# Optimization experiments

Measured on AMD Instinct MI355X. Metric: run time of the kernel, lower is better.

Reference implementation:

```python
import jax, jax.numpy as jnp
import numpy as np

DIM = 1024


def setup_inputs() -> dict:
    key = jax.random.key(0)
    ks = jax.random.split(key, 10)
    B, S, D = 8, 2048, DIM
    sd = 1.0 / np.sqrt(D)  # nn.Linear default init scale
    return {
        "query": jax.random.normal(ks[0], (B, S, D), jnp.float32),
        "key": jax.random.normal(ks[1], (B, S, D), jnp.float32),
        "value": jax.random.normal(ks[2], (B, S, D), jnp.float32),
        "context": jnp.zeros((D,), jnp.float32),
        "Wq": jax.random.uniform(ks[3], (D, D), jnp.float32, -sd, sd),
        "bq": jax.random.uniform(ks[4], (D,), jnp.float32, -sd, sd),
        "Wk": jax.random.uniform(ks[5], (D, D), jnp.float32, -sd, sd),
        "bk": jax.random.uniform(ks[6], (D,), jnp.float32, -sd, sd),
        "Wv": jax.random.uniform(ks[7], (D, D), jnp.float32, -sd, sd),
        "bv": jax.random.uniform(ks[8], (D,), jnp.float32, -sd, sd),
    }


def reference(query, key, value, context, Wq, bq, Wk, bk, Wv, bv):
    D = query.shape[-1]
    scale = D ** (-0.5)
    # context bias added to inputs BEFORE q/k projections (not v)
    q = jnp.einsum("bsd,ed->bse", query + context, Wq) + bq
    k = jnp.einsum("bsd,ed->bse", key + context, Wk) + bk
    v = jnp.einsum("bsd,ed->bse", value, Wv) + bv
    scores = jnp.einsum("bqd,bkd->bqk", q, k) * scale  # [B,S,S]
    S = scores.shape[-1]
    causal = jnp.triu(jnp.ones((S, S), jnp.bool_), k=1)  # True = masked
    scores = jnp.where(causal, -jnp.inf, scores)
    weights = jax.nn.softmax(scores, axis=-1)
    out = jnp.einsum("bqk,bkd->bqd", weights, v)
    return out
```

## Files before the change

kernel.cpp:

```cpp
#include <hip/hip_runtime.h>
#include <hip/hip_bf16.h>
#include <stdint.h>
#include <math.h>

#define DIM   1024
#define SEQ   2048
#define BATCH 8
#define BSD   (BATCH * SEQ * DIM)
#define DD    (DIM * DIM)

typedef __attribute__((ext_vector_type(8))) short short8;
typedef __attribute__((ext_vector_type(4))) float floatx4;
typedef unsigned int u32;
typedef unsigned short ushort_t;

#define GLOAD_LDS16(gptr, lptr)                                                   \
    __builtin_amdgcn_global_load_lds(                                             \
        (const __attribute__((address_space(1))) u32*)(gptr),                     \
        (__attribute__((address_space(3))) u32*)(lptr), 16, 0, 0)

__device__ __forceinline__ uint2 pack4bf(float a, float b, float c, float d) {
    union { __hip_bfloat162 h; unsigned u; } p0, p1;
    p0.h = __float22bfloat162_rn(float2{a, b});
    p1.h = __float22bfloat162_rn(float2{c, d});
    return uint2{p0.u, p1.u};
}

__global__ __launch_bounds__(256) void convert_kernel(
    const float* __restrict__ q, const float* __restrict__ k, const float* __restrict__ v,
    const float* __restrict__ ctx,
    const float* __restrict__ Wq, const float* __restrict__ Wk, const float* __restrict__ Wv,
    ushort_t* __restrict__ xq, ushort_t* __restrict__ xk, ushort_t* __restrict__ xv,
    ushort_t* __restrict__ wq, ushort_t* __restrict__ wk, ushort_t* __restrict__ wv)
{
    const long idx = (long)blockIdx.x * 256 + threadIdx.x;
    const long T  = BSD / 4;
    const long W4 = DD / 4;
    if (idx < 3 * T) {
        const int  seg = (int)(idx >> 22);
        const long off = idx & (T - 1);
        const float* src = (seg == 0) ? q : (seg == 1) ? k : v;
        ushort_t*    dst = (seg == 0) ? xq : (seg == 1) ? xk : xv;
        float4 x = ((const float4*)src)[off];
        if (seg < 2) {
            const float4 c = ((const float4*)ctx)[off & (DIM / 4 - 1)];
            x.x += c.x; x.y += c.y; x.z += c.z; x.w += c.w;
        }
        ((uint2*)dst)[off] = pack4bf(x.x, x.y, x.z, x.w);
    } else {
        const long r   = idx - 3 * T;
        const int  seg = (int)(r >> 18);
        const long off = r & (W4 - 1);
        const float* src = (seg == 0) ? Wq : (seg == 1) ? Wk : Wv;
        ushort_t*    dst = (seg == 0) ? wq : (seg == 1) ? wk : wv;
        const float4 x = ((const float4*)src)[off];
        ((uint2*)dst)[off] = pack4bf(x.x, x.y, x.z, x.w);
    }
}

__global__ __launch_bounds__(256) void gemm_bf16(
    const ushort_t* __restrict__ X, const ushort_t* __restrict__ W,
    const float* __restrict__ bias, ushort_t* __restrict__ out, int transpose_out)
{
    __shared__ ushort_t As[128 * 64];
    __shared__ ushort_t Bs[128 * 64];

    const int tid  = threadIdx.x;
    const int lane = tid & 63;
    const int wave = tid >> 6;
    const int quad = lane >> 4;
    const int l16  = lane & 15;
    const int wy = wave >> 1, wx = wave & 1;
    const int row0 = blockIdx.x * 128;
    const int col0 = blockIdx.y * 128;

    floatx4 acc[4][4];
#pragma unroll
    for (int i = 0; i < 4; ++i)
#pragma unroll
        for (int j = 0; j < 4; ++j)
            acc[i][j] = (floatx4){0.f, 0.f, 0.f, 0.f};

    const int srow = lane >> 3;
    const int scol = (lane & 7) * 8;

    for (int k0 = 0; k0 < DIM; k0 += 64) {
#pragma unroll
        for (int i = 0; i < 4; ++i) {
            const int slot = wave * 4 + i;
            const int grow = slot * 8 + srow;
            GLOAD_LDS16(&X[(size_t)(row0 + grow) * DIM + k0 + scol],
                        &As[slot * 512 + lane * 8]);
            GLOAD_LDS16(&W[(size_t)(col0 + grow) * DIM + k0 + scol],
                        &Bs[slot * 512 + lane * 8]);
        }
        __syncthreads();

        short8 af[4][2], bfr[4][2];
#pragma unroll
        for (int t = 0; t < 4; ++t)
#pragma unroll
            for (int ks = 0; ks < 2; ++ks) {
                af[t][ks]  = *(const short8*)&As[(wy * 64 + t * 16 + l16) * 64 + ks * 32 + quad * 8];
                bfr[t][ks] = *(const short8*)&Bs[(wx * 64 + t * 16 + l16) * 64 + ks * 32 + quad * 8];
            }
#pragma unroll
        for (int ks = 0; ks < 2; ++ks)
#pragma unroll
            for (int mt = 0; mt < 4; ++mt)
#pragma unroll
                for (int nt = 0; nt < 4; ++nt)
                    acc[mt][nt] = __builtin_amdgcn_mfma_f32_16x16x32_bf16(
                        af[mt][ks], bfr[nt][ks], acc[mt][nt], 0, 0, 0);
        __syncthreads();
    }

#pragma unroll
    for (int nt = 0; nt < 4; ++nt) {
        const int n = col0 + wx * 64 + nt * 16 + l16;
        const float bz = bias[n];
#pragma unroll
        for (int mt = 0; mt < 4; ++mt) {
            const int mbase = row0 + wy * 64 + mt * 16 + quad * 4;
            const floatx4 a = acc[mt][nt];
            if (!transpose_out) {
#pragma unroll
                for (int rg = 0; rg < 4; ++rg) {
                    union { __hip_bfloat16 h; ushort_t u; } cv;
                    cv.h = __float2bfloat16(a[rg] + bz);
                    out[(size_t)(mbase + rg) * DIM + n] = cv.u;
                }
            } else {
                const int bb = mbase >> 11;
                const int ss = mbase & (SEQ - 1);
                *(uint2*)&out[((size_t)bb * DIM + n) * SEQ + ss] =
                    pack4bf(a[0] + bz, a[1] + bz, a[2] + bz, a[3] + bz);
            }
        }
    }
}

__global__ __launch_bounds__(512, 2) void attn_kernel(
    const ushort_t* __restrict__ Q, const ushort_t* __restrict__ K,
    const ushort_t* __restrict__ VT, float* __restrict__ out)
{
    __shared__ float Sp[8 * 32 * 36];
    __shared__ ushort_t Pl[32 * 72];
    __shared__ float mS[32], lS[32], aS[32];

    const int tid  = threadIdx.x;
    const int lane = tid & 63;
    const int wave = tid >> 6;
    const int quad = lane >> 4;
    const int l16  = lane & 15;

    const int jt = wave >> 2;
    const int dq = wave & 3;
    const int d0 = dq * 256;

    const int by = blockIdx.x & 7;
    const int p  = blockIdx.x >> 3;

    const size_t qrow = (size_t)by * SEQ;
    const size_t vrow = (size_t)by * DIM;
    const int dchunk = wave * 128;

    const int rr  = tid >> 4;
    const int kt  = tid & 15;
    const int kk0 = kt * 4;
    const int sjt = kk0 >> 5;
    const int sc  = kk0 & 31;

    for (int pass = 0; pass < 2; ++pass) {
        const int t  = pass ? (63 - p) : p;
        const int q0 = t * 32;
        const int ngroups = (t + 2) >> 1;

        if (tid < 32) { mS[tid] = -INFINITY; lS[tid] = 0.f; aS[tid] = 0.f; }

        short8 qa[2][8];
#pragma unroll
        for (int mt = 0; mt < 2; ++mt)
#pragma unroll
            for (int ks = 0; ks < 8; ++ks)
                qa[mt][ks] = *(const short8*)
                    &Q[(qrow + q0 + mt * 16 + l16) * DIM + d0 + ks * 32 + quad * 8];

        floatx4 o[2][8];
#pragma unroll
        for (int mt = 0; mt < 2; ++mt)
#pragma unroll
            for (int nt = 0; nt < 8; ++nt)
                o[mt][nt] = (floatx4){0.f, 0.f, 0.f, 0.f};

        __syncthreads();

        for (int g = 0; g < ngroups; ++g) {
            const int k0 = g * 64 + jt * 32;

            floatx4 s00 = (floatx4){0.f,0.f,0.f,0.f}, s01 = s00, s10 = s00, s11 = s00;
            const ushort_t* kbp = &K[(qrow + k0 + l16) * DIM + d0 + quad * 8];
#pragma unroll
            for (int ks = 0; ks < 8; ++ks) {
                const short8 kb0 = *(const short8*)&kbp[ks * 32];
                const short8 kb1 = *(const short8*)&kbp[16 * DIM + ks * 32];
                s00 = __builtin_amdgcn_mfma_f32_16x16x32_bf16(qa[0][ks], kb0, s00, 0, 0, 0);
                s10 = __builtin_amdgcn_mfma_f32_16x16x32_bf16(qa[1][ks], kb0, s10, 0, 0, 0);
                s01 = __builtin_amdgcn_mfma_f32_16x16x32_bf16(qa[0][ks], kb1, s01, 0, 0, 0);
                s11 = __builtin_amdgcn_mfma_f32_16x16x32_bf16(qa[1][ks], kb1, s11, 0, 0, 0);
            }
#pragma unroll
            for (int rg = 0; rg < 4; ++rg) {
                const int r0 = quad * 4 + rg;
                Sp[(wave * 32 + r0) * 36 + l16]           = s00[rg];
                Sp[(wave * 32 + r0) * 36 + 16 + l16]      = s01[rg];
                Sp[(wave * 32 + 16 + r0) * 36 + l16]      = s10[rg];
                Sp[(wave * 32 + 16 + r0) * 36 + 16 + l16] = s11[rg];
            }
            __syncthreads();

            short8 vcur[8];
#pragma unroll
            for (int nt = 0; nt < 8; ++nt)
                vcur[nt] = *(const short8*)
                    &VT[(vrow + dchunk + nt * 16 + l16) * SEQ + g * 64 + quad * 8];

            float sv[4];
            {
                const float* a0 = &Sp[((sjt * 4 + 0) * 32 + rr) * 36 + sc];
                const float4 x0 = *(const float4*)&a0[0];
                const float4 x1 = *(const float4*)&a0[32 * 36];
                const float4 x2 = *(const float4*)&a0[2 * 32 * 36];
                const float4 x3 = *(const float4*)&a0[3 * 32 * 36];
                sv[0] = x0.x + x1.x + x2.x + x3.x;
                sv[1] = x0.y + x1.y + x2.y + x3.y;
                sv[2] = x0.z + x1.z + x2.z + x3.z;
                sv[3] = x0.w + x1.w + x2.w + x3.w;
            }
            const int rowg = q0 + rr;
#pragma unroll
            for (int i = 0; i < 4; ++i) {
                const int key = g * 64 + kk0 + i;
                sv[i] = (key > rowg) ? -INFINITY : sv[i] * 0.03125f;
            }
            float mx = fmaxf(fmaxf(sv[0], sv[1]), fmaxf(sv[2], sv[3]));
#pragma unroll
            for (int off = 1; off < 16; off <<= 1) mx = fmaxf(mx, __shfl_xor(mx, off));
            const float mold = mS[rr];
            const float mnew = fmaxf(mold, mx);
            const float p0 = __expf(sv[0] - mnew), p1 = __expf(sv[1] - mnew);
            const float p2 = __expf(sv[2] - mnew), p3 = __expf(sv[3] - mnew);
            float rs = (p0 + p1) + (p2 + p3);
#pragma unroll
            for (int off = 1; off < 16; off <<= 1) rs += __shfl_xor(rs, off);
            const float alpha = __expf(mold - mnew);
            if (kt == 0) {
                mS[rr] = mnew;
                lS[rr] = lS[rr] * alpha + rs;
                aS[rr] = alpha;
            }
            *(uint2*)&Pl[rr * 72 + kk0] = pack4bf(p0, p1, p2, p3);
            __syncthreads();

#pragma unroll
            for (int mt = 0; mt < 2; ++mt) {
                const float a0 = aS[mt * 16 + quad * 4 + 0];
                const float a1 = aS[mt * 16 + quad * 4 + 1];
                const float a2 = aS[mt * 16 + quad * 4 + 2];
                const float a3 = aS[mt * 16 + quad * 4 + 3];
#pragma unroll
                for (int nt = 0; nt < 8; ++nt) {
                    o[mt][nt][0] *= a0; o[mt][nt][1] *= a1;
                    o[mt][nt][2] *= a2; o[mt][nt][3] *= a3;
                }
            }
            {
                const short8 pa0 = *(const short8*)&Pl[l16 * 72 + quad * 8];
                const short8 pa1 = *(const short8*)&Pl[(16 + l16) * 72 + quad * 8];
#pragma unroll
                for (int nt = 0; nt < 8; ++nt) {
                    o[0][nt] = __builtin_amdgcn_mfma_f32_16x16x32_bf16(pa0, vcur[nt], o[0][nt], 0, 0, 0);
                    o[1][nt] = __builtin_amdgcn_mfma_f32_16x16x32_bf16(pa1, vcur[nt], o[1][nt], 0, 0, 0);
                }
            }
            {
                short8 vb[8];
#pragma unroll
                for (int nt = 0; nt < 8; ++nt)
                    vb[nt] = *(const short8*)
                        &VT[(vrow + dchunk + nt * 16 + l16) * SEQ + g * 64 + 32 + quad * 8];
                const short8 pa0 = *(const short8*)&Pl[l16 * 72 + 32 + quad * 8];
                const short8 pa1 = *(const short8*)&Pl[(16 + l16) * 72 + 32 + quad * 8];
#pragma unroll
                for (int nt = 0; nt < 8; ++nt) {
                    o[0][nt] = __builtin_amdgcn_mfma_f32_16x16x32_bf16(pa0, vb[nt], o[0][nt], 0, 0, 0);
                    o[1][nt] = __builtin_amdgcn_mfma_f32_16x16x32_bf16(pa1, vb[nt], o[1][nt], 0, 0, 0);
                }
            }
        }

#pragma unroll
        for (int mt = 0; mt < 2; ++mt) {
            const float li0 = 1.f / lS[mt * 16 + quad * 4 + 0];
            const float li1 = 1.f / lS[mt * 16 + quad * 4 + 1];
            const float li2 = 1.f / lS[mt * 16 + quad * 4 + 2];
            const float li3 = 1.f / lS[mt * 16 + quad * 4 + 3];
#pragma unroll
            for (int nt = 0; nt < 8; ++nt) {
                const size_t base = (qrow + q0 + mt * 16 + quad * 4) * DIM + wave * 128 + nt * 16 + l16;
                out[base]           = o[mt][nt][0] * li0;
                out[base + DIM]     = o[mt][nt][1] * li1;
                out[base + 2 * DIM] = o[mt][nt][2] * li2;
                out[base + 3 * DIM] = o[mt][nt][3] * li3;
            }
        }
        __syncthreads();
    }
}

extern "C" void kernel_launch(void* const* d_in, const int* in_sizes, int n_in,
                              void* d_out, int out_size, void* d_ws, size_t ws_size,
                              hipStream_t stream) {
    const float* query = (const float*)d_in[0];
    const float* key   = (const float*)d_in[1];
    const float* value = (const float*)d_in[2];
    const float* ctx   = (const float*)d_in[3];
    const float* Wq    = (const float*)d_in[4];
    const float* bq    = (const float*)d_in[5];
    const float* Wk    = (const float*)d_in[6];
    const float* bk    = (const float*)d_in[7];
    const float* Wv    = (const float*)d_in[8];
    const float* bv    = (const float*)d_in[9];

    ushort_t* A = (ushort_t*)d_ws;
    ushort_t* B = A + (size_t)BSD;
    ushort_t* C = B + (size_t)BSD;
    ushort_t* D = C + (size_t)BSD;
    ushort_t* wqb = D + (size_t)BSD;
    ushort_t* wkb = wqb + (size_t)DD;
    ushort_t* wvb = wkb + (size_t)DD;
    float* out = (float*)d_out;

    {
        const long total = 3L * (BSD / 4) + 3L * (DD / 4);
        convert_kernel<<<dim3((unsigned)(total / 256)), dim3(256), 0, stream>>>(
            query, key, value, ctx, Wq, Wk, Wv, A, B, C, wqb, wkb, wvb);
    }

    const dim3 pg((BATCH * SEQ) / 128, DIM / 128);
    gemm_bf16<<<pg, dim3(256), 0, stream>>>(C, wvb, bv, D, 1);
    gemm_bf16<<<pg, dim3(256), 0, stream>>>(A, wqb, bq, C, 0);
    gemm_bf16<<<pg, dim3(256), 0, stream>>>(B, wkb, bk, A, 0);

    attn_kernel<<<dim3(BATCH * (SEQ / 64)), dim3(512), 0, stream>>>(C, A, D, out);
}
```

Measured before the change: 674.6 us.

## Split QK^T over all waves by head-dim and prefetch next K tile into registers

Each wave now computes the full 32x64 score tile over its own 128-wide slice of the head dimension, instead of a 32x32 half over a 256-wide slice. The eight partial tiles are summed through a larger LDS buffer. The K fragments for the next key group are loaded into a second register buffer, alternating between two buffers, while the current group runs, so global load latency overlaps with compute. The cost is more register pressure from the two 4x4 short8 K buffers under launch_bounds(512,2), plus twice the LDS reduction reads and a larger Sp array.

New measurement: 1.335 ms. 1.98x slower.

```diff
diff --git a/kernel.cpp b/kernel.cpp
--- a/kernel.cpp
+++ b/kernel.cpp
@@ -140,11 +140,114 @@
     }
 }
 
+#define ATTN_GROUP(G, KC, KN)                                                      \
+    {                                                                              \
+        floatx4 s[2][4];                                                           \
+        _Pragma("unroll")                                                          \
+        for (int mt = 0; mt < 2; ++mt)                                             \
+            _Pragma("unroll")                                                      \
+            for (int kf = 0; kf < 4; ++kf)                                         \
+                s[mt][kf] = (floatx4){0.f, 0.f, 0.f, 0.f};                         \
+        _Pragma("unroll")                                                          \
+        for (int ks = 0; ks < 4; ++ks)                                             \
+            _Pragma("unroll")                                                      \
+            for (int kf = 0; kf < 4; ++kf) {                                       \
+                s[0][kf] = __builtin_amdgcn_mfma_f32_16x16x32_bf16(qa[0][ks], KC[kf][ks], s[0][kf], 0, 0, 0); \
+                s[1][kf] = __builtin_amdgcn_mfma_f32_16x16x32_bf16(qa[1][ks], KC[kf][ks], s[1][kf], 0, 0, 0); \
+            }                                                                      \
+        _Pragma("unroll")                                                          \
+        for (int kf = 0; kf < 4; ++kf)                                             \
+            _Pragma("unroll")                                                      \
+            for (int rg = 0; rg < 4; ++rg) {                                       \
+                const int r0 = quad * 4 + rg;                                      \
+                Sp[(wave * 32 + r0) * 68 + kf * 16 + l16]      = s[0][kf][rg];     \
+                Sp[(wave * 32 + 16 + r0) * 68 + kf * 16 + l16] = s[1][kf][rg];     \
+            }                                                                      \
+        if ((G) + 1 < ngroups) {                                                   \
+            const ushort_t* knp = &K[(qrow + ((G) + 1) * 64 + l16) * DIM + d0 + quad * 8]; \
+            _Pragma("unroll")                                                      \
+            for (int kf = 0; kf < 4; ++kf)                                         \
+                _Pragma("unroll")                                                  \
+                for (int ks = 0; ks < 4; ++ks)                                     \
+                    KN[kf][ks] = *(const short8*)&knp[(size_t)kf * 16 * DIM + ks * 32]; \
+        }                                                                          \
+        __syncthreads();                                                           \
+        short8 vcur[8];                                                            \
+        _Pragma("unroll")                                                          \
+        for (int nt = 0; nt < 8; ++nt)                                             \
+            vcur[nt] = *(const short8*)&VT[(vrow + d0 + nt * 16 + l16) * SEQ + (G) * 64 + quad * 8]; \
+        float sv[4];                                                               \
+        {                                                                          \
+            const float* ap = &Sp[rr * 68 + kk0];                                  \
+            float4 acc4 = *(const float4*)&ap[0];                                  \
+            _Pragma("unroll")                                                      \
+            for (int w = 1; w < 8; ++w) {                                          \
+                const float4 x = *(const float4*)&ap[w * 32 * 68];                 \
+                acc4.x += x.x; acc4.y += x.y; acc4.z += x.z; acc4.w += x.w;        \
+            }                                                                      \
+            sv[0] = acc4.x; sv[1] = acc4.y; sv[2] = acc4.z; sv[3] = acc4.w;        \
+        }                                                                          \
+        const int rowg = q0 + rr;                                                  \
+        _Pragma("unroll")                                                          \
+        for (int i = 0; i < 4; ++i) {                                              \
+            const int key = (G) * 64 + kk0 + i;                                    \
+            sv[i] = (key > rowg) ? -INFINITY : sv[i] * 0.03125f;                   \
+        }                                                                          \
+        float mx = fmaxf(fmaxf(sv[0], sv[1]), fmaxf(sv[2], sv[3]));                \
+        _Pragma("unroll")                                                          \
+        for (int off = 1; off < 16; off <<= 1) mx = fmaxf(mx, __shfl_xor(mx, off)); \
+        const float mold = mS[rr];                                                 \
+        const float mnew = fmaxf(mold, mx);                                        \
+        const float p0 = __expf(sv[0] - mnew), p1 = __expf(sv[1] - mnew);          \
+        const float p2 = __expf(sv[2] - mnew), p3 = __expf(sv[3] - mnew);          \
+        float rsum = (p0 + p1) + (p2 + p3);                                        \
+        _Pragma("unroll")                                                          \
+        for (int off = 1; off < 16; off <<= 1) rsum += __shfl_xor(rsum, off);      \
+        const float alpha = __expf(mold - mnew);                                   \
+        if (kt == 0) { mS[rr] = mnew; lS[rr] = lS[rr] * alpha + rsum; aS[rr] = alpha; } \
+        *(uint2*)&Pl[rr * 72 + kk0] = pack4bf(p0, p1, p2, p3);                     \
+        __syncthreads();                                                           \
+        _Pragma("unroll")                                                          \
+        for (int mt = 0; mt < 2; ++mt) {                                           \
+            const float a0r = aS[mt * 16 + quad * 4 + 0];                          \
+            const float a1r = aS[mt * 16 + quad * 4 + 1];                          \
+            const float a2r = aS[mt * 16 + quad * 4 + 2];                          \
+            const float a3r = aS[mt * 16 + quad * 4 + 3];                          \
+            _Pragma("unroll")                                                      \
+            for (int nt = 0; nt < 8; ++nt) {                                       \
+                o[mt][nt][0] *= a0r; o[mt][nt][1] *= a1r;                          \
+                o[mt][nt][2] *= a2r; o[mt][nt][3] *= a3r;                          \
+            }                                                                      \
+        }                                                                          \
+        {                                                                          \
+            const short8 pa0 = *(const short8*)&Pl[l16 * 72 + quad * 8];           \
+            const short8 pa1 = *(const short8*)&Pl[(16 + l16) * 72 + quad * 8];    \
+            _Pragma("unroll")                                                      \
+            for (int nt = 0; nt < 8; ++nt) {                                       \
+                o[0][nt] = __builtin_amdgcn_mfma_f32_16x16x32_bf16(pa0, vcur[nt], o[0][nt], 0, 0, 0); \
+                o[1][nt] = __builtin_amdgcn_mfma_f32_16x16x32_bf16(pa1, vcur[nt], o[1][nt], 0, 0, 0); \
+            }                                                                      \
+        }                                                                          \
+        {                                                                          \
+            short8 vb[8];                                                          \
+            _Pragma("unroll")                                                      \
+            for (int nt = 0; nt < 8; ++nt)                                         \
+                vb[nt] = *(const short8*)&VT[(vrow + d0 + nt * 16 + l16) * SEQ + (G) * 64 + 32 + quad * 8]; \
+            const short8 pb0 = *(const short8*)&Pl[l16 * 72 + 32 + quad * 8];      \
+            const short8 pb1 = *(const short8*)&Pl[(16 + l16) * 72 + 32 + quad * 8]; \
+            _Pragma("unroll")                                                      \
+            for (int nt = 0; nt < 8; ++nt) {                                       \
+                o[0][nt] = __builtin_amdgcn_mfma_f32_16x16x32_bf16(pb0, vb[nt], o[0][nt], 0, 0, 0); \
+                o[1][nt] = __builtin_amdgcn_mfma_f32_16x16x32_bf16(pb1, vb[nt], o[1][nt], 0, 0, 0); \
+            }                                                                      \
+        }                                                                          \
+    }
+
 __global__ __launch_bounds__(512, 2) void attn_kernel(
     const ushort_t* __restrict__ Q, const ushort_t* __restrict__ K,
     const ushort_t* __restrict__ VT, float* __restrict__ out)
 {
-    __shared__ float Sp[8 * 32 * 36];
+    __shared__ float Sp[8 * 32 * 68];
     __shared__ ushort_t Pl[32 * 72];
     __shared__ float mS[32], lS[32], aS[32];
 
@@ -153,23 +256,17 @@
     const int wave = tid >> 6;
     const int quad = lane >> 4;
     const int l16  = lane & 15;
-
-    const int jt = wave >> 2;
-    const int dq = wave & 3;
-    const int d0 = dq * 256;
+    const int d0   = wave * 128;
 
     const int by = blockIdx.x & 7;
     const int p  = blockIdx.x >> 3;
 
     const size_t qrow = (size_t)by * SEQ;
     const size_t vrow = (size_t)by * DIM;
-    const int dchunk = wave * 128;
 
     const int rr  = tid >> 4;
     const int kt  = tid & 15;
     const int kk0 = kt * 4;
-    const int sjt = kk0 >> 5;
-    const int sc  = kk0 & 31;
 
     for (int pass = 0; pass < 2; ++pass) {
         const int t  = pass ? (63 - p) : p;
@@ -178,11 +275,11 @@
 
         if (tid < 32) { mS[tid] = -INFINITY; lS[tid] = 0.f; aS[tid] = 0.f; }
 
-        short8 qa[2][8];
+        short8 qa[2][4];
 #pragma unroll
         for (int mt = 0; mt < 2; ++mt)
 #pragma unroll
-            for (int ks = 0; ks < 8; ++ks)
+            for (int ks = 0; ks < 4; ++ks)
                 qa[mt][ks] = *(const short8*)
                     &Q[(qrow + q0 + mt * 16 + l16) * DIM + d0 + ks * 32 + quad * 8];
 
@@ -193,110 +290,21 @@
             for (int nt = 0; nt < 8; ++nt)
                 o[mt][nt] = (floatx4){0.f, 0.f, 0.f, 0.f};
 
+        short8 kA[4][4], kB[4][4];
+        {
+            const ushort_t* kp = &K[(qrow + l16) * DIM + d0 + quad * 8];
+#pragma unroll
+            for (int kf = 0; kf < 4; ++kf)
+#pragma unroll
+                for (int ks = 0; ks < 4; ++ks)
+                    kA[kf][ks] = *(const short8*)&kp[(size_t)kf * 16 * DIM + ks * 32];
+        }
+
         __syncthreads();
 
         for (int g = 0; g < ngroups; ++g) {
-            const int k0 = g * 64 + jt * 32;
-
-            floatx4 s00 = (floatx4){0.f,0.f,0.f,0.f}, s01 = s00, s10 = s00, s11 = s00;
-            const ushort_t* kbp = &K[(qrow + k0 + l16) * DIM + d0 + quad * 8];
-#pragma unroll
-            for (int ks = 0; ks < 8; ++ks) {
-                const short8 kb0 = *(const short8*)&kbp[ks * 32];
-                const short8 kb1 = *(const short8*)&kbp[16 * DIM + ks * 32];
-                s00 = __builtin_amdgcn_mfma_f32_16x16x32_bf16(qa[0][ks], kb0, s00, 0, 0, 0);
-                s10 = __builtin_amdgcn_mfma_f32_16x16x32_bf16(qa[1][ks], kb0, s10, 0, 0, 0);
-                s01 = __builtin_amdgcn_mfma_f32_16x16x32_bf16(qa[0][ks], kb1, s01, 0, 0, 0);
-                s11 = __builtin_amdgcn_mfma_f32_16x16x32_bf16(qa[1][ks], kb1, s11, 0, 0, 0);
-            }
-#pragma unroll
-            for (int rg = 0; rg < 4; ++rg) {
-                const int r0 = quad * 4 + rg;
-                Sp[(wave * 32 + r0) * 36 + l16]           = s00[rg];
-                Sp[(wave * 32 + r0) * 36 + 16 + l16]      = s01[rg];
-                Sp[(wave * 32 + 16 + r0) * 36 + l16]      = s10[rg];
-                Sp[(wave * 32 + 16 + r0) * 36 + 16 + l16] = s11[rg];
-            }
-            __syncthreads();
-
-            short8 vcur[8];
-#pragma unroll
-            for (int nt = 0; nt < 8; ++nt)
-                vcur[nt] = *(const short8*)
-                    &VT[(vrow + dchunk + nt * 16 + l16) * SEQ + g * 64 + quad * 8];
-
-            float sv[4];
-            {
-                const float* a0 = &Sp[((sjt * 4 + 0) * 32 + rr) * 36 + sc];
-                const float4 x0 = *(const float4*)&a0[0];
-                const float4 x1 = *(const float4*)&a0[32 * 36];
-                const float4 x2 = *(const float4*)&a0[2 * 32 * 36];
-                const float4 x3 = *(const float4*)&a0[3 * 32 * 36];
-                sv[0] = x0.x + x1.x + x2.x + x3.x;
-                sv[1] = x0.y + x1.y + x2.y + x3.y;
-                sv[2] = x0.z + x1.z + x2.z + x3.z;
-                sv[3] = x0.w + x1.w + x2.w + x3.w;
-            }
-            const int rowg = q0 + rr;
-#pragma unroll
-            for (int i = 0; i < 4; ++i) {
-                const int key = g * 64 + kk0 + i;
-                sv[i] = (key > rowg) ? -INFINITY : sv[i] * 0.03125f;
-            }
-            float mx = fmaxf(fmaxf(sv[0], sv[1]), fmaxf(sv[2], sv[3]));
-#pragma unroll
-            for (int off = 1; off < 16; off <<= 1) mx = fmaxf(mx, __shfl_xor(mx, off));
-            const float mold = mS[rr];
-            const float mnew = fmaxf(mold, mx);
-            const float p0 = __expf(sv[0] - mnew), p1 = __expf(sv[1] - mnew);
-            const float p2 = __expf(sv[2] - mnew), p3 = __expf(sv[3] - mnew);
-            float rs = (p0 + p1) + (p2 + p3);
-#pragma unroll
-            for (int off = 1; off < 16; off <<= 1) rs += __shfl_xor(rs, off);
-            const float alpha = __expf(mold - mnew);
-            if (kt == 0) {
-                mS[rr] = mnew;
-                lS[rr] = lS[rr] * alpha + rs;
-                aS[rr] = alpha;
-            }
-            *(uint2*)&Pl[rr * 72 + kk0] = pack4bf(p0, p1, p2, p3);
-            __syncthreads();
-
-#pragma unroll
-            for (int mt = 0; mt < 2; ++mt) {
-                const float a0 = aS[mt * 16 + quad * 4 + 0];
-                const float a1 = aS[mt * 16 + quad * 4 + 1];
-                const float a2 = aS[mt * 16 + quad * 4 + 2];
-                const float a3 = aS[mt * 16 + quad * 4 + 3];
-#pragma unroll
-                for (int nt = 0; nt < 8; ++nt) {
-                    o[mt][nt][0] *= a0; o[mt][nt][1] *= a1;
-                    o[mt][nt][2] *= a2; o[mt][nt][3] *= a3;
-                }
-            }
-            {
-                const short8 pa0 = *(const short8*)&Pl[l16 * 72 + quad * 8];
-                const short8 pa1 = *(const short8*)&Pl[(16 + l16) * 72 + quad * 8];
-#pragma unroll
-                for (int nt = 0; nt < 8; ++nt) {
-                    o[0][nt] = __builtin_amdgcn_mfma_f32_16x16x32_bf16(pa0, vcur[nt], o[0][nt], 0, 0, 0);
-                    o[1][nt] = __builtin_amdgcn_mfma_f32_16x16x32_bf16(pa1, vcur[nt], o[1][nt], 0, 0, 0);
-                }
-            }
-            {
-                short8 vb[8];
-#pragma unroll
-                for (int nt = 0; nt < 8; ++nt)
-                    vb[nt] = *(const short8*)
-                        &VT[(vrow + dchunk + nt * 16 + l16) * SEQ + g * 64 + 32 + quad * 8];
-                const short8 pa0 = *(const short8*)&Pl[l16 * 72 + 32 + quad * 8];
-                const short8 pa1 = *(const short8*)&Pl[(16 + l16) * 72 + 32 + quad * 8];
-#pragma unroll
-                for (int nt = 0; nt < 8; ++nt) {
-                    o[0][nt] = __builtin_amdgcn_mfma_f32_16x16x32_bf16(pa0, vb[nt], o[0][nt], 0, 0, 0);
-                    o[1][nt] = __builtin_amdgcn_mfma_f32_16x16x32_bf16(pa1, vb[nt], o[1][nt], 0, 0, 0);
-                }
-            }
+            if ((g & 1) == 0) ATTN_GROUP(g, kA, kB)
+            else              ATTN_GROUP(g, kB, kA)
         }
 
 #pragma unroll
@@ -307,7 +315,7 @@
             const float li3 = 1.f / lS[mt * 16 + quad * 4 + 3];
 #pragma unroll
             for (int nt = 0; nt < 8; ++nt) {
-                const size_t base = (qrow + q0 + mt * 16 + quad * 4) * DIM + wave * 128 + nt * 16 + l16;
+                const size_t base = (qrow + q0 + mt * 16 + quad * 4) * DIM + d0 + nt * 16 + l16;
                 out[base]           = o[mt][nt][0] * li0;
                 out[base + DIM]     = o[mt][nt][1] * li1;
                 out[base + 2 * DIM] = o[mt][nt][2] * li2;
```
